# Kernel tuning notes

Hardware: AMD Instinct MI355X
Metric: run time of the kernel (lower is better)

The kernel has to match this reference:

```python
import jax, jax.numpy as jnp
import numpy as np

ENC_H = 512
DEC_H = 512
FIELD = 128

def setup_inputs() -> dict:
    key = jax.random.key(0)
    ks = jax.random.split(key, 12)
    B, S, T = 8, 256, 32
    def lin(k, fan_in, fan_out):
        k1, k2 = jax.random.split(k)
        bound = 1.0 / np.sqrt(fan_in)
        W = jax.random.uniform(k1, (fan_in, fan_out), minval=-bound, maxval=bound, dtype=jnp.float32)
        b = jax.random.uniform(k2, (fan_out,), minval=-bound, maxval=bound, dtype=jnp.float32)
        return W, b
    W1, b1 = lin(ks[0], ENC_H, DEC_H)
    W2, b2 = lin(ks[1], DEC_H, DEC_H)
    W3, b3 = lin(ks[2], FIELD, DEC_H)
    W4, b4 = lin(ks[3], DEC_H, DEC_H)
    return {
        "output": jax.random.normal(ks[4], (B, T, DEC_H), dtype=jnp.float32),
        "encoder_hidden": jax.random.normal(ks[5], (S, B, ENC_H), dtype=jnp.float32),
        "input_z": jax.random.normal(ks[6], (B, S, FIELD), dtype=jnp.float32),
        "W1": W1, "b1": b1, "W2": W2, "b2": b2,
        "W3": W3, "b3": b3, "W4": W4, "b4": b4,
    }

def reference(output, encoder_hidden, input_z, W1, b1, W2, b2, W3, b3, W4, b4):
    S, B, He = encoder_hidden.shape
    # tanh(lin1(encoder_hidden)) then .view(B, S, D)  (reshape, NOT transpose -- faithful to torch .view)
    out_hs = jnp.tanh(encoder_hidden @ W1 + b1).reshape(B, S, -1)      # [B,S,D]
    enc_h = encoder_hidden.reshape(B, S, He)                            # [B,S,He]
    out_fds = jnp.tanh(input_z @ W3 + b3)                               # [B,S,D]
    out2 = jnp.tanh(output @ W2 + b2)                                   # [B,T,D]
    out3 = jnp.tanh(output @ W4 + b4)                                   # [B,T,D]
    # vectorized over timesteps: g1[b,s,t,d] = out_hs[b,s,d]*out2[b,t,d]
    g1 = out_hs[:, :, None, :] * out2[:, None, :, :]                    # [B,S,T,D]
    alpha = jax.nn.softmax(g1, axis=1)                                  # softmax over S, per feature d
    g2 = out_fds[:, :, None, :] * out3[:, None, :, :]                   # [B,S,T,D]
    beta = jax.nn.softmax(g2, axis=1)
    q = alpha * beta                                                    # [B,S,T,D]
    qn = jax.lax.stop_gradient(jnp.sum(q, axis=1, keepdims=True))       # detached normalizer
    gamma = q / qn                                                      # [B,S,T,D]
    contex = jnp.sum(gamma * enc_h[:, :, None, :], axis=1)              # [B,T,D]
    concat_vectors = jnp.concatenate([output, contex], axis=-1)         # [B,T,2D]
    # attn: list over t of gamma[:, :, t, :] -> stacked [B,T,S,D]
    attn = jnp.transpose(gamma, (0, 2, 1, 3))
    return (concat_vectors, attn)
```

## Files before the change

### kernel.cpp

```cpp
#include <hip/hip_runtime.h>


typedef __attribute__((ext_vector_type(8))) short bf16x8;
typedef __attribute__((ext_vector_type(4))) float f32x4;

__device__ __forceinline__ unsigned short f2bf(float x) {
    union { float f; unsigned u; } v; v.f = x;
    unsigned r = v.u + 0x7fffu + ((v.u >> 16) & 1u);
    return (unsigned short)(r >> 16);
}

__global__ __launch_bounds__(256) void cvt_all_k(
    const float* __restrict__ E, const float* __restrict__ Z, const float* __restrict__ O,
    unsigned short* __restrict__ Ebf, unsigned short* __restrict__ Zbf, unsigned short* __restrict__ Obf)
{
    int b = blockIdx.x;
    const float* src; unsigned short* dst; int base;
    if (b < 1024)      { src = E; dst = Ebf; base = b; }
    else if (b < 1280) { src = Z; dst = Zbf; base = b - 1024; }
    else               { src = O; dst = Obf; base = b - 1280; }
    int i = base * 1024 + threadIdx.x * 4;
    float4 v = *(const float4*)(src + i);
    ushort4 r;
    r.x = f2bf(v.x); r.y = f2bf(v.y); r.z = f2bf(v.z); r.w = f2bf(v.w);
    *(ushort4*)(dst + i) = r;
}

__global__ __launch_bounds__(256) void transpose_all_k(
    const float* __restrict__ W1, const float* __restrict__ W2,
    const float* __restrict__ W3, const float* __restrict__ W4,
    unsigned short* __restrict__ W1T, unsigned short* __restrict__ W2T,
    unsigned short* __restrict__ W3T, unsigned short* __restrict__ W4T)
{
    const float* W; unsigned short* WT; int K;
    switch (blockIdx.z) {
      case 0:  W = W1; WT = W1T; K = 512; break;
      case 1:  W = W2; WT = W2T; K = 512; break;
      case 2:  W = W3; WT = W3T; K = 128; break;
      default: W = W4; WT = W4T; K = 512; break;
    }
    int k0 = blockIdx.y * 32;
    if (k0 >= K) return;
    int n0 = blockIdx.x * 32;
    __shared__ float tile[32][33];
    int tx = threadIdx.x, ty = threadIdx.y;
    #pragma unroll
    for (int i = 0; i < 32; i += 8)
        tile[ty + i][tx] = W[(k0 + ty + i) * 512 + n0 + tx];
    __syncthreads();
    #pragma unroll
    for (int i = 0; i < 32; i += 8)
        WT[(n0 + ty + i) * K + k0 + tx] = f2bf(tile[tx][ty + i]);
}

__global__ __launch_bounds__(256) void gemm_all_k(
    const unsigned short* __restrict__ Ebf, const unsigned short* __restrict__ Zbf,
    const unsigned short* __restrict__ Obf,
    const unsigned short* __restrict__ W1T, const unsigned short* __restrict__ W3T,
    const unsigned short* __restrict__ W2T, const unsigned short* __restrict__ W4T,
    const float* __restrict__ b1, const float* __restrict__ b3,
    const float* __restrict__ b2, const float* __restrict__ b4,
    float* __restrict__ L1, float* __restrict__ F,
    float* __restrict__ O2, float* __restrict__ O3)
{
    const unsigned short* A; const unsigned short* BT; const float* bias; float* C;
    int M, K;
    switch (blockIdx.z) {
      case 0:  A = Ebf; BT = W1T; bias = b1; C = L1; M = 2048; K = 512; break;
      case 1:  A = Zbf; BT = W3T; bias = b3; C = F;  M = 2048; K = 128; break;
      case 2:  A = Obf; BT = W2T; bias = b2; C = O2; M = 256;  K = 512; break;
      default: A = Obf; BT = W4T; bias = b4; C = O3; M = 256;  K = 512; break;
    }
    int m0 = blockIdx.x * 64;
    if (m0 >= M) return;
    int n0 = blockIdx.y * 64;

    __shared__ unsigned short As[64 * 40];
    __shared__ unsigned short Bs[64 * 40];

    int tid  = threadIdx.x;
    int wave = tid >> 6;
    int lane = tid & 63;
    int lm   = lane & 15;
    int lq   = lane >> 4;

    int srow = tid >> 2;
    int scol = (tid & 3) * 8;

    f32x4 acc[4];
    #pragma unroll
    for (int c = 0; c < 4; ++c) acc[c] = f32x4{0.f, 0.f, 0.f, 0.f};

    for (int k0 = 0; k0 < K; k0 += 32) {
        __syncthreads();
        *(uint4*)(&As[srow * 40 + scol]) = *(const uint4*)(&A[(m0 + srow) * K + k0 + scol]);
        *(uint4*)(&Bs[srow * 40 + scol]) = *(const uint4*)(&BT[(n0 + srow) * K + k0 + scol]);
        __syncthreads();
        bf16x8 af = *(const bf16x8*)(&As[(wave * 16 + lm) * 40 + lq * 8]);
        #pragma unroll
        for (int c = 0; c < 4; ++c) {
            bf16x8 bfr = *(const bf16x8*)(&Bs[(c * 16 + lm) * 40 + lq * 8]);
            acc[c] = __builtin_amdgcn_mfma_f32_16x16x32_bf16(af, bfr, acc[c], 0, 0, 0);
        }
    }

    #pragma unroll
    for (int c = 0; c < 4; ++c) {
        int col = n0 + c * 16 + lm;
        float bv = bias[col];
        #pragma unroll
        for (int r = 0; r < 4; ++r) {
            int row = m0 + wave * 16 + lq * 4 + r;
            float x = acc[c][r] + bv;
            x = fminf(fmaxf(x, -15.f), 15.f);
            float t = __expf(2.0f * x);
            C[row * 512 + col] = (t - 1.0f) / (t + 1.0f);
        }
    }
}

__global__ __launch_bounds__(256) void attn_k(
    const float* __restrict__ L1, const float* __restrict__ F,
    const float* __restrict__ O2, const float* __restrict__ O3,
    const float* __restrict__ Enc, const float* __restrict__ Out,
    float* __restrict__ out0, float* __restrict__ attn)
{
    int bt = blockIdx.x;
    int d  = blockIdx.y * 256 + threadIdx.x;
    int b  = bt >> 5;

    float c2 = O2[bt * 512 + d];
    float c3 = O3[bt * 512 + d];
    const float* L1b = L1  + (b * 256) * 512 + d;
    const float* Fb  = F   + (b * 256) * 512 + d;
    const float* Eb  = Enc + (b * 256) * 512 + d;

    float sum = 0.f, csum = 0.f;
    #pragma unroll 8
    for (int s = 0; s < 256; ++s) {
        float z = L1b[s * 512] * c2 + Fb[s * 512] * c3;
        float e = __expf(z);
        sum  += e;
        csum += e * Eb[s * 512];
    }
    float inv = 1.0f / sum;

    out0[bt * 1024 + d]       = Out[bt * 512 + d];
    out0[bt * 1024 + 512 + d] = csum * inv;

    float* ap = attn + (bt * 256) * 512 + d;
    #pragma unroll 8
    for (int s = 0; s < 256; ++s) {
        float z = L1b[s * 512] * c2 + Fb[s * 512] * c3;
        ap[s * 512] = __expf(z) * inv;
    }
}

extern "C" void kernel_launch(void* const* d_in, const int* in_sizes, int n_in,
                              void* d_out, int out_size, void* d_ws, size_t ws_size,
                              hipStream_t stream)
{
    const float* Out = (const float*)d_in[0];
    const float* Enc = (const float*)d_in[1];
    const float* Z   = (const float*)d_in[2];
    const float* W1  = (const float*)d_in[3];
    const float* b1  = (const float*)d_in[4];
    const float* W2  = (const float*)d_in[5];
    const float* b2  = (const float*)d_in[6];
    const float* W3  = (const float*)d_in[7];
    const float* b3  = (const float*)d_in[8];
    const float* W4  = (const float*)d_in[9];
    const float* b4  = (const float*)d_in[10];

    char* ws = (char*)d_ws;
    size_t off = 0;
    auto alloc = [&](size_t n) -> char* {
        char* p = ws + off; off += (n + 255) & ~(size_t)255; return p;
    };
    unsigned short* Ebf = (unsigned short*)alloc(1048576 * 2);
    unsigned short* Zbf = (unsigned short*)alloc(262144 * 2);
    unsigned short* Obf = (unsigned short*)alloc(131072 * 2);
    unsigned short* W1T = (unsigned short*)alloc(262144 * 2);
    unsigned short* W2T = (unsigned short*)alloc(262144 * 2);
    unsigned short* W3T = (unsigned short*)alloc(65536 * 2);
    unsigned short* W4T = (unsigned short*)alloc(262144 * 2);
    float* L1 = (float*)alloc(1048576 * 4);
    float* F  = (float*)alloc(1048576 * 4);
    float* O2 = (float*)alloc(131072 * 4);
    float* O3 = (float*)alloc(131072 * 4);

    float* out0 = (float*)d_out;
    float* attn = out0 + 262144;

    hipLaunchKernelGGL(cvt_all_k, dim3(1408), dim3(256), 0, stream,
                       Enc, Z, Out, Ebf, Zbf, Obf);
    hipLaunchKernelGGL(transpose_all_k, dim3(16, 16, 4), dim3(32, 8), 0, stream,
                       W1, W2, W3, W4, W1T, W2T, W3T, W4T);
    hipLaunchKernelGGL(gemm_all_k, dim3(32, 8, 4), dim3(256), 0, stream,
                       Ebf, Zbf, Obf, W1T, W3T, W2T, W4T,
                       b1, b3, b2, b4, L1, F, O2, O3);
    hipLaunchKernelGGL(attn_k, dim3(256, 2), dim3(256), 0, stream,
                       L1, F, O2, O3, Enc, Out, out0, attn);
}
```

Measured before the change: 207.0 us.

## Split attention into S-chunked partial reductions, finalize, and vectorized attn write

Replaces the single attention kernel, which launched only 512 blocks and streamed each s row serially, with three kernels. The first computes partial softmax sums over S chunks and reuses each loaded L1/F/Enc value across 16 timesteps. The second reduces the partials and writes the context and inverse normalizer. The third writes the large attn tensor with float4 stores, loading L1/F once per block and looping over t. This adds parallelism and register-level reuse, at the cost of two extra launches and partial buffers in the workspace.

```diff
diff --git a/kernel.cpp b/kernel.cpp
--- a/kernel.cpp
+++ b/kernel.cpp
@@ -119,40 +119,106 @@
     }
 }
 
-__global__ __launch_bounds__(256) void attn_k(
+__global__ __launch_bounds__(256) void attn_partial_k(
     const float* __restrict__ L1, const float* __restrict__ F,
     const float* __restrict__ O2, const float* __restrict__ O3,
-    const float* __restrict__ Enc, const float* __restrict__ Out,
-    float* __restrict__ out0, float* __restrict__ attn)
+    const float* __restrict__ Enc,
+    float* __restrict__ sum_p, float* __restrict__ csum_p)
+{
+    int b  = blockIdx.x >> 3;
+    int sc = blockIdx.x & 7;
+    int tc = blockIdx.y;
+    int dc = blockIdx.z;
+    int d  = dc * 256 + threadIdx.x;
+
+    float c2[16], c3[16], sum[16], csum[16];
+    #pragma unroll
+    for (int i = 0; i < 16; ++i) {
+        int bt = b * 32 + tc * 16 + i;
+        c2[i] = O2[bt * 512 + d];
+        c3[i] = O3[bt * 512 + d];
+        sum[i] = 0.f; csum[i] = 0.f;
+    }
+
+    int s0 = sc * 32;
+    const float* L1b = L1  + (b * 256 + s0) * 512 + d;
+    const float* Fb  = F   + (b * 256 + s0) * 512 + d;
+    const float* Eb  = Enc + (b * 256 + s0) * 512 + d;
+
+    #pragma unroll 2
+    for (int s = 0; s < 32; ++s) {
+        float l1 = L1b[s * 512];
+        float f  = Fb[s * 512];
+        float eh = Eb[s * 512];
+        #pragma unroll
+        for (int i = 0; i < 16; ++i) {
+            float e = __expf(l1 * c2[i] + f * c3[i]);
+            sum[i]  += e;
+            csum[i] += e * eh;
+        }
+    }
+
+    #pragma unroll
+    for (int i = 0; i < 16; ++i) {
+        int idx = ((b * 8 + sc) * 32 + tc * 16 + i) * 512 + d;
+        sum_p[idx]  = sum[i];
+        csum_p[idx] = csum[i];
+    }
+}
+
+__global__ __launch_bounds__(256) void attn_finalize_k(
+    const float* __restrict__ sum_p, const float* __restrict__ csum_p,
+    const float* __restrict__ Out,
+    float* __restrict__ out0, float* __restrict__ invA)
 {
     int bt = blockIdx.x;
     int d  = blockIdx.y * 256 + threadIdx.x;
-    int b  = bt >> 5;
-
-    float c2 = O2[bt * 512 + d];
-    float c3 = O3[bt * 512 + d];
-    const float* L1b = L1  + (b * 256) * 512 + d;
-    const float* Fb  = F   + (b * 256) * 512 + d;
-    const float* Eb  = Enc + (b * 256) * 512 + d;
+    int b  = bt >> 5, t = bt & 31;
 
     float sum = 0.f, csum = 0.f;
-    #pragma unroll 8
-    for (int s = 0; s < 256; ++s) {
-        float z = L1b[s * 512] * c2 + Fb[s * 512] * c3;
-        float e = __expf(z);
-        sum  += e;
-        csum += e * Eb[s * 512];
+    #pragma unroll
+    for (int sc = 0; sc < 8; ++sc) {
+        int idx = ((b * 8 + sc) * 32 + t) * 512 + d;
+        sum  += sum_p[idx];
+        csum += csum_p[idx];
     }
     float inv = 1.0f / sum;
-
+    invA[bt * 512 + d] = inv;
     out0[bt * 1024 + d]       = Out[bt * 512 + d];
     out0[bt * 1024 + 512 + d] = csum * inv;
-
-    float* ap = attn + (bt * 256) * 512 + d;
-    #pragma unroll 8
-    for (int s = 0; s < 256; ++s) {
-        float z = L1b[s * 512] * c2 + Fb[s * 512] * c3;
-        ap[s * 512] = __expf(z) * inv;
+}
+
+__global__ __launch_bounds__(256) void attn_write_k(
+    const float* __restrict__ L1, const float* __restrict__ F,
+    const float* __restrict__ O2, const float* __restrict__ O3,
+    const float* __restrict__ invA,
+    float* __restrict__ attn)
+{
+    int b  = blockIdx.x;
+    int s0 = blockIdx.y * 4 + ((threadIdx.x >> 7) * 2);
+    int d4 = (threadIdx.x & 127) * 4;
+
+    float4 l1[2], f[2];
+    #pragma unroll
+    for (int j = 0; j < 2; ++j) {
+        l1[j] = *(const float4*)(L1 + (b * 256 + s0 + j) * 512 + d4);
+        f[j]  = *(const float4*)(F  + (b * 256 + s0 + j) * 512 + d4);
+    }
+
+    for (int t = 0; t < 32; ++t) {
+        int bt = b * 32 + t;
+        float4 c2 = *(const float4*)(O2   + bt * 512 + d4);
+        float4 c3 = *(const float4*)(O3   + bt * 512 + d4);
+        float4 iv = *(const float4*)(invA + bt * 512 + d4);
+        #pragma unroll
+        for (int j = 0; j < 2; ++j) {
+            float4 g;
+            g.x = __expf(l1[j].x * c2.x + f[j].x * c3.x) * iv.x;
+            g.y = __expf(l1[j].y * c2.y + f[j].y * c3.y) * iv.y;
+            g.z = __expf(l1[j].z * c2.z + f[j].z * c3.z) * iv.z;
+            g.w = __expf(l1[j].w * c2.w + f[j].w * c3.w) * iv.w;
+            *(float4*)(attn + ((size_t)(bt * 256 + s0 + j)) * 512 + d4) = g;
+        }
     }
 }
 
@@ -184,10 +250,13 @@
     unsigned short* W2T = (unsigned short*)alloc(262144 * 2);
     unsigned short* W3T = (unsigned short*)alloc(65536 * 2);
     unsigned short* W4T = (unsigned short*)alloc(262144 * 2);
-    float* L1 = (float*)alloc(1048576 * 4);
-    float* F  = (float*)alloc(1048576 * 4);
-    float* O2 = (float*)alloc(131072 * 4);
-    float* O3 = (float*)alloc(131072 * 4);
+    float* L1    = (float*)alloc(1048576 * 4);
+    float* F     = (float*)alloc(1048576 * 4);
+    float* O2    = (float*)alloc(131072 * 4);
+    float* O3    = (float*)alloc(131072 * 4);
+    float* sum_p = (float*)alloc(1048576 * 4);
+    float* csum_p= (float*)alloc(1048576 * 4);
+    float* invA  = (float*)alloc(131072 * 4);
 
     float* out0 = (float*)d_out;
     float* attn = out0 + 262144;
@@ -199,6 +268,10 @@
     hipLaunchKernelGGL(gemm_all_k, dim3(32, 8, 4), dim3(256), 0, stream,
                        Ebf, Zbf, Obf, W1T, W3T, W2T, W4T,
                        b1, b3, b2, b4, L1, F, O2, O3);
-    hipLaunchKernelGGL(attn_k, dim3(256, 2), dim3(256), 0, stream,
-                       L1, F, O2, O3, Enc, Out, out0, attn);
-}
+    hipLaunchKernelGGL(attn_partial_k, dim3(64, 2, 2), dim3(256), 0, stream,
+                       L1, F, O2, O3, Enc, sum_p, csum_p);
+    hipLaunchKernelGGL(attn_finalize_k, dim3(256, 2), dim3(256), 0, stream,
+                       sum_p, csum_p, Out, out0, invA);
+    hipLaunchKernelGGL(attn_write_k, dim3(8, 64), dim3(256), 0, stream,
+                       L1, F, O2, O3, invA, attn);
+}
```

New measurement: 206.6 us. Within noise of the previous version (-0.2%).
